# Optimization experiments

Measured on AMD Instinct MI355X. Metric: run time of the kernel, lower is better.

## Reference

```python
import jax, jax.numpy as jnp
import numpy as np

N, D, E, H, O, K = 4096, 1024, 8, 2048, 1024, 2
LOSS_COEF = 0.01


def setup_inputs() -> dict:
    key = jax.random.key(0)
    ks = jax.random.split(key, 8)
    x = jax.random.normal(ks[0], (N, D), jnp.float32)
    return {
        "x": x,
        "x_offsets": jnp.array([0, N // 2, N], jnp.int32),  # unused by forward math
        "max_seq_len": 2048,
        "group_norm": False,
        "num_groups": 8,
        "linear_dim": D // 8,
        "norm_weight": jax.random.uniform(ks[1], (D,), jnp.float32, 0.5, 1.5),
        "norm_bias": jax.random.normal(ks[2], (D,), jnp.float32) * 0.1,
        "norm_eps": 1e-5,
        "w_gate": jax.random.normal(ks[3], (D, E), jnp.float32) * (1.0 / np.sqrt(D)),
        "experts_hidden_w": jax.random.normal(ks[4], (E, H, D), jnp.float32) * 0.02,
        "experts_hidden_bias": jnp.zeros((E, H), jnp.float32),
        "experts_w": jax.random.normal(ks[5], (E, O, H), jnp.float32) * 0.02,
        "experts_bias": jnp.zeros((E, O), jnp.float32),
        "output_weight": jax.random.normal(ks[6], (D, O), jnp.float32) * 0.02,
    }


def _cv_squared(v, eps=1e-6):
    v = v.astype(jnp.float32)
    m = v.mean()
    return jnp.var(v, ddof=1) / (m * m + eps)  # torch .var() is unbiased


def reference(x, x_offsets, max_seq_len, group_norm, num_groups, linear_dim,
              norm_weight, norm_bias, norm_eps,
              w_gate, experts_hidden_w, experts_hidden_bias,
              experts_w, experts_bias, output_weight):
    # ---- input normalization (layer_norm branch; group_norm=False) ----
    if group_norm:
        xg = x.reshape(-1, num_groups, linear_dim)
        mu = xg.mean(axis=2, keepdims=True)
        var = ((xg - mu) ** 2).mean(axis=2, keepdims=True)
        xg = (xg - mu) * jax.lax.rsqrt(var + norm_eps)
        xg = xg * norm_weight[None, :, None] + norm_bias[None, :, None]
        x_norm = xg.reshape(-1, x.shape[-1])
    else:
        mu = x.mean(axis=-1, keepdims=True)
        var = ((x - mu) ** 2).mean(axis=-1, keepdims=True)  # biased, like F.layer_norm
        x_norm = (x - mu) * jax.lax.rsqrt(var + norm_eps) * norm_weight + norm_bias

    # ---- gating: clean logits (enable_noisy_gating=False), L2-normalize rows ----
    logits = x_norm @ w_gate                                  # [N, E]
    logits = logits / jnp.maximum(
        jnp.linalg.norm(logits, axis=1, keepdims=True), 1e-12)
    probs = jax.nn.softmax(logits, axis=1)                    # softmax over all experts
    _, top_idx = jax.lax.top_k(logits, K)                     # [N, K]
    gates_k = jnp.take_along_axis(probs, top_idx, axis=1)     # top-k of softmax(logits)
    rows = jnp.arange(logits.shape[0])[:, None]
    gates = jnp.zeros_like(logits).at[rows, top_idx].set(gates_k)  # [N, E] sparse gates

    # ---- load-balancing loss (train=True, non-noisy path) ----
    importance = gates.sum(axis=0)
    load = (gates > 0).sum(axis=0).astype(jnp.float32)
    loss = (_cv_squared(importance) + _cv_squared(load)) * LOSS_COEF

    # ---- expert MLPs; gates are exactly zero off top-k so masked-dense == dispatch ----
    h = jax.nn.silu(jnp.einsum('nd,ehd->enh', x_norm, experts_hidden_w)
                    + experts_hidden_bias[:, None, :])        # [E, N, H]
    eo = jnp.einsum('enh,eoh->eno', h, experts_w) + experts_bias[:, None, :]  # [E, N, O]
    y_moe = jnp.einsum('ne,eno->no', gates.astype(jnp.float32),
                       eo.astype(jnp.float32))                # fp32 combine, like index_add

    # ---- residual projection: addmm(y_moe, x, output_weight) ----
    y = y_moe + x @ output_weight
    gate_fraction = load / load.sum()
    return (y, loss, gate_fraction)
```

## Files before the change

kernel.cpp:

```cpp
#include <hip/hip_runtime.h>
#include <hip/hip_bf16.h>
#include <stdint.h>

#define N_TOK 4096
#define DIM   1024
#define NE    8
#define NH    2048
#define NO    1024

typedef __attribute__((ext_vector_type(8))) short bf16x8;
typedef __attribute__((ext_vector_type(16))) float f32x16;

__device__ inline unsigned short f2bf(float f) {
    unsigned u = __float_as_uint(f);
    u += 0x7fffu + ((u >> 16) & 1u);
    return (unsigned short)(u >> 16);
}

__device__ inline void async_copy16(const void* g, void* l) {
    __builtin_amdgcn_global_load_lds(
        (const __attribute__((address_space(1))) void*)g,
        (__attribute__((address_space(3))) void*)l, 16, 0, 0);
}

__global__ __launch_bounds__(256) void ln_gate_kernel(
    const float* __restrict__ x, const float* __restrict__ nw,
    const float* __restrict__ nb, const float* __restrict__ eps_p,
    const float* __restrict__ wg,
    unsigned short* __restrict__ xn_bf, unsigned short* __restrict__ x_bf,
    int* __restrict__ tok_e, float* __restrict__ tok_g)
{
    int n = blockIdx.x;
    int t = threadIdx.x;
    int lane = t & 63, wv = t >> 6;

    const float4 xv = ((const float4*)(x + (size_t)n * DIM))[t];
    float s  = xv.x + xv.y + xv.z + xv.w;
    float s2 = xv.x*xv.x + xv.y*xv.y + xv.z*xv.z + xv.w*xv.w;
    #pragma unroll
    for (int o = 32; o > 0; o >>= 1) {
        s  += __shfl_down(s, o);
        s2 += __shfl_down(s2, o);
    }
    __shared__ float rs[4], rs2[4];
    __shared__ float gred[4][NE];
    if (lane == 0) { rs[wv] = s; rs2[wv] = s2; }
    __syncthreads();
    float S  = rs[0] + rs[1] + rs[2] + rs[3];
    float S2 = rs2[0] + rs2[1] + rs2[2] + rs2[3];
    const float inv = 1.0f / (float)DIM;
    float mu = S * inv;
    float var = fmaxf(S2 * inv - mu * mu, 0.0f);
    float rstd = rsqrtf(var + eps_p[0]);

    float4 w4 = ((const float4*)nw)[t];
    float4 b4 = ((const float4*)nb)[t];
    float xn0 = (xv.x - mu) * rstd * w4.x + b4.x;
    float xn1 = (xv.y - mu) * rstd * w4.y + b4.y;
    float xn2 = (xv.z - mu) * rstd * w4.z + b4.z;
    float xn3 = (xv.w - mu) * rstd * w4.w + b4.w;

    ushort4 pn; pn.x = f2bf(xn0); pn.y = f2bf(xn1); pn.z = f2bf(xn2); pn.w = f2bf(xn3);
    ((ushort4*)(xn_bf + (size_t)n * DIM))[t] = pn;
    ushort4 px; px.x = f2bf(xv.x); px.y = f2bf(xv.y); px.z = f2bf(xv.z); px.w = f2bf(xv.w);
    ((ushort4*)(x_bf + (size_t)n * DIM))[t] = px;

    float acc[NE];
    #pragma unroll
    for (int e = 0; e < NE; ++e) acc[e] = 0.0f;
    float xns[4] = {xn0, xn1, xn2, xn3};
    const float4* wgp = (const float4*)(wg + (size_t)(4 * t) * NE);
    #pragma unroll
    for (int j = 0; j < 4; ++j) {
        float4 w0 = wgp[2 * j], w1 = wgp[2 * j + 1];
        float xj = xns[j];
        acc[0] += xj * w0.x; acc[1] += xj * w0.y; acc[2] += xj * w0.z; acc[3] += xj * w0.w;
        acc[4] += xj * w1.x; acc[5] += xj * w1.y; acc[6] += xj * w1.z; acc[7] += xj * w1.w;
    }
    #pragma unroll
    for (int o = 32; o > 0; o >>= 1) {
        #pragma unroll
        for (int e = 0; e < NE; ++e) acc[e] += __shfl_down(acc[e], o);
    }
    if (lane == 0) {
        #pragma unroll
        for (int e = 0; e < NE; ++e) gred[wv][e] = acc[e];
    }
    __syncthreads();
    if (t == 0) {
        float lg[NE];
        float nrm2 = 0.0f;
        #pragma unroll
        for (int e = 0; e < NE; ++e) {
            lg[e] = gred[0][e] + gred[1][e] + gred[2][e] + gred[3][e];
            nrm2 += lg[e] * lg[e];
        }
        float den = fmaxf(sqrtf(nrm2), 1e-12f);
        float linv = 1.0f / den;
        #pragma unroll
        for (int e = 0; e < NE; ++e) lg[e] *= linv;
        float mx = lg[0];
        #pragma unroll
        for (int e = 1; e < NE; ++e) mx = fmaxf(mx, lg[e]);
        float p[NE], ps = 0.0f;
        #pragma unroll
        for (int e = 0; e < NE; ++e) { p[e] = expf(lg[e] - mx); ps += p[e]; }
        float pinv = 1.0f / ps;
        #pragma unroll
        for (int e = 0; e < NE; ++e) p[e] *= pinv;
        int i0 = 0; float b0 = lg[0];
        #pragma unroll
        for (int e = 1; e < NE; ++e) if (lg[e] > b0) { b0 = lg[e]; i0 = e; }
        int i1 = -1; float b1 = -3.0e38f;
        #pragma unroll
        for (int e = 0; e < NE; ++e) if (e != i0 && lg[e] > b1) { b1 = lg[e]; i1 = e; }
        tok_e[2 * n] = i0; tok_e[2 * n + 1] = i1;
        tok_g[2 * n] = p[i0]; tok_g[2 * n + 1] = p[i1];
    }
}

__global__ void cvt2_bf16_kernel(const float* __restrict__ a, unsigned short* __restrict__ da,
                                 const float* __restrict__ b, unsigned short* __restrict__ db,
                                 int n4each) {
    int i = blockIdx.x * blockDim.x + threadIdx.x;
    const float4* s; ushort4* d; int j;
    if (i < n4each) { s = (const float4*)a; d = (ushort4*)da; j = i; }
    else            { s = (const float4*)b; d = (ushort4*)db; j = i - n4each; }
    float4 v = s[j];
    ushort4 o; o.x = f2bf(v.x); o.y = f2bf(v.y); o.z = f2bf(v.z); o.w = f2bf(v.w);
    d[j] = o;
}

__global__ void transpose_cvt_kernel(const float* __restrict__ w,
                                     unsigned short* __restrict__ wt) {
    __shared__ float tile[32][33];
    int tx = threadIdx.x, ty = threadIdx.y;
    int o0 = blockIdx.x * 32, d0 = blockIdx.y * 32;
    tile[ty][tx] = w[(size_t)(d0 + ty) * NO + o0 + tx];
    __syncthreads();
    wt[(size_t)(o0 + ty) * DIM + d0 + tx] = f2bf(tile[tx][ty]);
}

__device__ inline float cv_sq(const float* v) {
    float m = 0.0f;
    for (int e = 0; e < NE; ++e) m += v[e];
    m *= (1.0f / NE);
    float s = 0.0f;
    for (int e = 0; e < NE; ++e) { float d = v[e] - m; s += d * d; }
    s *= (1.0f / (NE - 1));
    return s / (m * m + 1e-6f);
}

__global__ __launch_bounds__(256) void route_kernel(
    const int* __restrict__ tok_e, const float* __restrict__ tok_g,
    int* __restrict__ counts, int* __restrict__ offsets,
    int* __restrict__ rowsbuf, int* __restrict__ pair_slot,
    float* __restrict__ out_tail)
{
    int b = blockIdx.x, t = threadIdx.x;
    int lane = t & 63, wv = t >> 6;
    int chunk0 = b * 1024;

    int lc[NE]; float li[NE];
    #pragma unroll
    for (int e = 0; e < NE; ++e) { lc[e] = 0; li[e] = 0.0f; }
    int base = t * 32;
    #pragma unroll
    for (int q = 0; q < 8; ++q) {
        int4 e4 = *(const int4*)(tok_e + base + q * 4);
        float4 g4 = *(const float4*)(tok_g + base + q * 4);
        lc[e4.x]++; li[e4.x] += g4.x;
        lc[e4.y]++; li[e4.y] += g4.y;
        lc[e4.z]++; li[e4.z] += g4.z;
        lc[e4.w]++; li[e4.w] += g4.w;
    }
    int prior_flag = (base + 32 <= chunk0) ? 1 : 0;
    int lp[NE];
    #pragma unroll
    for (int e = 0; e < NE; ++e) lp[e] = prior_flag ? lc[e] : 0;

    #pragma unroll
    for (int o = 32; o > 0; o >>= 1) {
        #pragma unroll
        for (int e = 0; e < NE; ++e) {
            lc[e] += __shfl_down(lc[e], o);
            lp[e] += __shfl_down(lp[e], o);
            li[e] += __shfl_down(li[e], o);
        }
    }
    __shared__ int   sc[4][NE], sp[4][NE];
    __shared__ float sf[4][NE];
    __shared__ int   lcur[NE];
    if (lane == 0) {
        #pragma unroll
        for (int e = 0; e < NE; ++e) { sc[wv][e] = lc[e]; sp[wv][e] = lp[e]; sf[wv][e] = li[e]; }
    }
    __syncthreads();
    if (t == 0) {
        int cnt[NE], pri[NE]; float imp[NE];
        for (int e = 0; e < NE; ++e) {
            cnt[e] = sc[0][e] + sc[1][e] + sc[2][e] + sc[3][e];
            pri[e] = sp[0][e] + sp[1][e] + sp[2][e] + sp[3][e];
            imp[e] = sf[0][e] + sf[1][e] + sf[2][e] + sf[3][e];
        }
        int off = 0;
        for (int e = 0; e < NE; ++e) {
            lcur[e] = off + pri[e];
            if (b == 0) { counts[e] = cnt[e]; offsets[e] = off; }
            off += cnt[e];
        }
        if (b == 0) {
            float lcf[NE], lif[NE];
            for (int e = 0; e < NE; ++e) { lcf[e] = (float)cnt[e]; lif[e] = imp[e]; }
            float tot = (float)off;
            out_tail[0] = 0.01f * (cv_sq(lif) + cv_sq(lcf));
            for (int e = 0; e < NE; ++e) out_tail[1 + e] = lcf[e] / tot;
        }
    }
    __syncthreads();

    int g0 = chunk0 + 4 * t;
    int4 e4 = *(const int4*)(tok_e + g0);
    int s0 = atomicAdd(&lcur[e4.x], 1);
    int s1 = atomicAdd(&lcur[e4.y], 1);
    int s2 = atomicAdd(&lcur[e4.z], 1);
    int s3 = atomicAdd(&lcur[e4.w], 1);
    int tok0 = g0 >> 1;
    rowsbuf[s0] = tok0;     rowsbuf[s1] = tok0;
    rowsbuf[s2] = tok0 + 1; rowsbuf[s3] = tok0 + 1;
    *(int4*)(pair_slot + g0) = (int4){s0, s1, s2, s3};
}

#define BK 64

__global__ __launch_bounds__(256) void gemm1_kernel(
    const unsigned short* __restrict__ xn,
    const unsigned short* __restrict__ wh,
    const float* __restrict__ hb,
    const int* __restrict__ rowsbuf,
    const int* __restrict__ counts, const int* __restrict__ offsets,
    unsigned short* __restrict__ hbuf)
{
    int e = blockIdx.z;
    int count = counts[e];
    int tm = blockIdx.y, tn = blockIdx.x;
    if (tm * 128 >= count) return;
    int off = offsets[e];

    __shared__ alignas(16) short As[128 * BK];
    __shared__ alignas(16) short Bs[128 * BK];

    int t = threadIdx.x;
    int c = t & 7, rl = t >> 3;
    int csw = (c ^ (rl & 7)) * 8;
    const unsigned short* aptr[4];
    const unsigned short* bptr[4];
    #pragma unroll
    for (int p = 0; p < 4; ++p) {
        int mrow = tm * 128 + p * 32 + rl;
        int mc = mrow < count ? mrow : count - 1;
        int token = rowsbuf[off + mc];
        aptr[p] = xn + (size_t)token * DIM;
        bptr[p] = wh + ((size_t)e * NH + tn * 128 + p * 32 + rl) * DIM;
    }

    int lane = t & 63, wvi = t >> 6;
    int wm = (wvi & 1) * 64, wn = (wvi >> 1) * 64;
    int l31 = lane & 31, h = lane >> 5, sw = l31 & 7;

    f32x16 acc[2][2];
    #pragma unroll
    for (int i = 0; i < 2; ++i)
        #pragma unroll
        for (int j = 0; j < 2; ++j) acc[i][j] = (f32x16)(0.0f);

    for (int kt = 0; kt < DIM / BK; ++kt) {
        int kb = kt * BK + csw;
        #pragma unroll
        for (int p = 0; p < 4; ++p)
            async_copy16(aptr[p] + kb, (char*)As + p * 4096 + t * 16);
        #pragma unroll
        for (int p = 0; p < 4; ++p)
            async_copy16(bptr[p] + kb, (char*)Bs + p * 4096 + t * 16);
        __syncthreads();
        #pragma unroll
        for (int ks = 0; ks < 4; ++ks) {
            int ph = ((ks * 2 + h) ^ sw) * 8;
            bf16x8 af[2], bfr[2];
            #pragma unroll
            for (int i = 0; i < 2; ++i)
                af[i] = *(const bf16x8*)&As[(wm + i * 32 + l31) * BK + ph];
            #pragma unroll
            for (int j = 0; j < 2; ++j)
                bfr[j] = *(const bf16x8*)&Bs[(wn + j * 32 + l31) * BK + ph];
            #pragma unroll
            for (int i = 0; i < 2; ++i)
                #pragma unroll
                for (int j = 0; j < 2; ++j)
                    acc[i][j] = __builtin_amdgcn_mfma_f32_32x32x16_bf16(af[i], bfr[j], acc[i][j], 0, 0, 0);
        }
        __syncthreads();
    }

    #pragma unroll
    for (int i = 0; i < 2; ++i) {
        #pragma unroll
        for (int j = 0; j < 2; ++j) {
            int col = tn * 128 + wn + j * 32 + l31;
            float bias = hb[e * NH + col];
            #pragma unroll
            for (int r = 0; r < 16; ++r) {
                int row_d = (r & 3) + 8 * (r >> 2) + 4 * h;
                int m = tm * 128 + wm + i * 32 + row_d;
                if (m < count) {
                    float v = acc[i][j][r] + bias;
                    v = v / (1.0f + __expf(-v));
                    hbuf[(size_t)(off + m) * NH + col] = f2bf(v);
                }
            }
        }
    }
}

__global__ __launch_bounds__(256) void gemm2_kernel(
    const unsigned short* __restrict__ hbuf,
    const unsigned short* __restrict__ wo,
    const float* __restrict__ ob,
    const int* __restrict__ counts, const int* __restrict__ offsets,
    float* __restrict__ eo)
{
    int e = blockIdx.z;
    int count = counts[e];
    int tm = blockIdx.y, tn = blockIdx.x;
    if (tm * 128 >= count) return;
    int off = offsets[e];

    __shared__ alignas(16) short As[128 * BK];
    __shared__ alignas(16) short Bs[64 * BK];

    int t = threadIdx.x;
    int c = t & 7, rl = t >> 3;
    int csw = (c ^ (rl & 7)) * 8;
    const unsigned short* aptr[4];
    const unsigned short* bptr[2];
    #pragma unroll
    for (int p = 0; p < 4; ++p) {
        int mrow = tm * 128 + p * 32 + rl;
        int mc = mrow < count ? mrow : count - 1;
        aptr[p] = hbuf + (size_t)(off + mc) * NH;
    }
    #pragma unroll
    for (int p = 0; p < 2; ++p)
        bptr[p] = wo + ((size_t)e * NO + tn * 64 + p * 32 + rl) * NH;

    int lane = t & 63, wvi = t >> 6;
    int wm = (wvi & 1) * 64, wn = (wvi >> 1) * 32;
    int l31 = lane & 31, h = lane >> 5, sw = l31 & 7;

    f32x16 acc[2];
    #pragma unroll
    for (int i = 0; i < 2; ++i) acc[i] = (f32x16)(0.0f);

    for (int kt = 0; kt < NH / BK; ++kt) {
        int kb = kt * BK + csw;
        #pragma unroll
        for (int p = 0; p < 4; ++p)
            async_copy16(aptr[p] + kb, (char*)As + p * 4096 + t * 16);
        #pragma unroll
        for (int p = 0; p < 2; ++p)
            async_copy16(bptr[p] + kb, (char*)Bs + p * 4096 + t * 16);
        __syncthreads();
        #pragma unroll
        for (int ks = 0; ks < 4; ++ks) {
            int ph = ((ks * 2 + h) ^ sw) * 8;
            bf16x8 af[2], bfr;
            #pragma unroll
            for (int i = 0; i < 2; ++i)
                af[i] = *(const bf16x8*)&As[(wm + i * 32 + l31) * BK + ph];
            bfr = *(const bf16x8*)&Bs[(wn + l31) * BK + ph];
            #pragma unroll
            for (int i = 0; i < 2; ++i)
                acc[i] = __builtin_amdgcn_mfma_f32_32x32x16_bf16(af[i], bfr, acc[i], 0, 0, 0);
        }
        __syncthreads();
    }

    int col = tn * 64 + wn + l31;
    float bias = ob[e * NO + col];
    #pragma unroll
    for (int i = 0; i < 2; ++i) {
        #pragma unroll
        for (int r = 0; r < 16; ++r) {
            int row_d = (r & 3) + 8 * (r >> 2) + 4 * h;
            int m = tm * 128 + wm + i * 32 + row_d;
            if (m < count)
                eo[(size_t)(off + m) * NO + col] = acc[i][r] + bias;
        }
    }
}

__global__ __launch_bounds__(256) void gemm_res_kernel(
    const unsigned short* __restrict__ xb,
    const unsigned short* __restrict__ wt,
    float* __restrict__ y)
{
    int tm = blockIdx.y, tn = blockIdx.x;
    __shared__ alignas(16) short As[64 * BK];
    __shared__ alignas(16) short Bs[128 * BK];

    int t = threadIdx.x;
    int c = t & 7, rl = t >> 3;
    int csw = (c ^ (rl & 7)) * 8;
    const unsigned short* aptr[2];
    const unsigned short* bptr[4];
    #pragma unroll
    for (int p = 0; p < 2; ++p)
        aptr[p] = xb + (size_t)(tm * 64 + p * 32 + rl) * DIM;
    #pragma unroll
    for (int p = 0; p < 4; ++p)
        bptr[p] = wt + (size_t)(tn * 128 + p * 32 + rl) * DIM;

    int lane = t & 63, wvi = t >> 6;
    int wm = (wvi & 1) * 32, wn = (wvi >> 1) * 64;
    int l31 = lane & 31, h = lane >> 5, sw = l31 & 7;

    f32x16 acc[2];
    #pragma unroll
    for (int j = 0; j < 2; ++j) acc[j] = (f32x16)(0.0f);

    for (int kt = 0; kt < DIM / BK; ++kt) {
        int kb = kt * BK + csw;
        #pragma unroll
        for (int p = 0; p < 2; ++p)
            async_copy16(aptr[p] + kb, (char*)As + p * 4096 + t * 16);
        #pragma unroll
        for (int p = 0; p < 4; ++p)
            async_copy16(bptr[p] + kb, (char*)Bs + p * 4096 + t * 16);
        __syncthreads();
        #pragma unroll
        for (int ks = 0; ks < 4; ++ks) {
            int ph = ((ks * 2 + h) ^ sw) * 8;
            bf16x8 af, bfr[2];
            af = *(const bf16x8*)&As[(wm + l31) * BK + ph];
            #pragma unroll
            for (int j = 0; j < 2; ++j)
                bfr[j] = *(const bf16x8*)&Bs[(wn + j * 32 + l31) * BK + ph];
            #pragma unroll
            for (int j = 0; j < 2; ++j)
                acc[j] = __builtin_amdgcn_mfma_f32_32x32x16_bf16(af, bfr[j], acc[j], 0, 0, 0);
        }
        __syncthreads();
    }

    #pragma unroll
    for (int j = 0; j < 2; ++j) {
        int col = tn * 128 + wn + j * 32 + l31;
        #pragma unroll
        for (int r = 0; r < 16; ++r) {
            int row_d = (r & 3) + 8 * (r >> 2) + 4 * h;
            int row = tm * 64 + wm + row_d;
            y[(size_t)row * NO + col] = acc[j][r];
        }
    }
}

__global__ __launch_bounds__(256) void combine_kernel(
    float* __restrict__ y, const float* __restrict__ eo,
    const int* __restrict__ pair_slot, const float* __restrict__ tok_g)
{
    int n = blockIdx.x, t = threadIdx.x;
    int s0 = pair_slot[2 * n], s1 = pair_slot[2 * n + 1];
    float g0 = tok_g[2 * n], g1 = tok_g[2 * n + 1];
    float4 a = ((const float4*)(eo + (size_t)s0 * NO))[t];
    float4 b = ((const float4*)(eo + (size_t)s1 * NO))[t];
    float4* yp = (float4*)(y + (size_t)n * NO) + t;
    float4 v = *yp;
    v.x += g0 * a.x + g1 * b.x;
    v.y += g0 * a.y + g1 * b.y;
    v.z += g0 * a.z + g1 * b.z;
    v.w += g0 * a.w + g1 * b.w;
    *yp = v;
}

extern "C" void kernel_launch(void* const* d_in, const int* in_sizes, int n_in,
                              void* d_out, int out_size, void* d_ws, size_t ws_size,
                              hipStream_t stream) {
    const float* x    = (const float*)d_in[0];
    const float* nw   = (const float*)d_in[6];
    const float* nb   = (const float*)d_in[7];
    const float* eps  = (const float*)d_in[8];
    const float* wg   = (const float*)d_in[9];
    const float* whw  = (const float*)d_in[10];
    const float* whb  = (const float*)d_in[11];
    const float* wow  = (const float*)d_in[12];
    const float* wob  = (const float*)d_in[13];
    const float* wout = (const float*)d_in[14];

    char* ws = (char*)d_ws;
    unsigned short* xn_bf = (unsigned short*)(ws + 0);
    unsigned short* x_bf  = (unsigned short*)(ws + 8388608);
    unsigned short* wh_bf = (unsigned short*)(ws + 16777216);
    float*          eo    = (float*)(ws + 16777216);
    unsigned short* wo_bf = (unsigned short*)(ws + 50331648);
    unsigned short* wt_bf = (unsigned short*)(ws + 83886080);
    unsigned short* hbuf  = (unsigned short*)(ws + 85983232);
    char* meta = ws + 119537664;
    int*   counts     = (int*)(meta + 0);
    int*   offsets    = (int*)(meta + 128);
    int*   tok_e      = (int*)(meta + 2048);
    float* tok_g      = (float*)(meta + 2048 + 32768);
    int*   rowsbuf    = (int*)(meta + 2048 + 65536);
    int*   pair_slot  = (int*)(meta + 2048 + 98304);

    float* y = (float*)d_out;
    float* out_tail = y + (size_t)N_TOK * NO;

    ln_gate_kernel<<<N_TOK, 256, 0, stream>>>(x, nw, nb, eps, wg, xn_bf, x_bf,
                                              tok_e, tok_g);
    {
        int n4 = NE * NH * DIM / 4;
        cvt2_bf16_kernel<<<2 * n4 / 256, 256, 0, stream>>>(whw, wh_bf, wow, wo_bf, n4);
    }
    transpose_cvt_kernel<<<dim3(NO / 32, DIM / 32), dim3(32, 32), 0, stream>>>(wout, wt_bf);
    route_kernel<<<NE, 256, 0, stream>>>(tok_e, tok_g, counts, offsets,
                                         rowsbuf, pair_slot, out_tail);
    gemm1_kernel<<<dim3(NH / 128, N_TOK / 128, NE), 256, 0, stream>>>(
        xn_bf, wh_bf, whb, rowsbuf, counts, offsets, hbuf);
    gemm2_kernel<<<dim3(NO / 64, N_TOK / 128, NE), 256, 0, stream>>>(
        hbuf, wo_bf, wob, counts, offsets, eo);
    gemm_res_kernel<<<dim3(NO / 128, N_TOK / 64), 256, 0, stream>>>(x_bf, wt_bf, y);
    combine_kernel<<<N_TOK, 256, 0, stream>>>(y, eo, pair_slot, tok_g);
}
```

Measured before the change: 389.1 us.

## Fuse prep kernels and scatter gated expert outputs via atomics into y

Merges the weight conversion, transpose, and routing kernels into one prep launch. Moves the residual GEMM ahead of the expert GEMMs so that gemm2 can add gate-weighted outputs straight into y with float atomics. This removes the fp32 eo buffer round trip and the separate combine kernel. The cost is 8M scattered atomic adds, and the fp32 summation order becomes nondeterministic.

```diff
diff --git a/kernel.cpp b/kernel.cpp
--- a/kernel.cpp
+++ b/kernel.cpp
@@ -119,28 +119,6 @@
     }
 }
 
-__global__ void cvt2_bf16_kernel(const float* __restrict__ a, unsigned short* __restrict__ da,
-                                 const float* __restrict__ b, unsigned short* __restrict__ db,
-                                 int n4each) {
-    int i = blockIdx.x * blockDim.x + threadIdx.x;
-    const float4* s; ushort4* d; int j;
-    if (i < n4each) { s = (const float4*)a; d = (ushort4*)da; j = i; }
-    else            { s = (const float4*)b; d = (ushort4*)db; j = i - n4each; }
-    float4 v = s[j];
-    ushort4 o; o.x = f2bf(v.x); o.y = f2bf(v.y); o.z = f2bf(v.z); o.w = f2bf(v.w);
-    d[j] = o;
-}
-
-__global__ void transpose_cvt_kernel(const float* __restrict__ w,
-                                     unsigned short* __restrict__ wt) {
-    __shared__ float tile[32][33];
-    int tx = threadIdx.x, ty = threadIdx.y;
-    int o0 = blockIdx.x * 32, d0 = blockIdx.y * 32;
-    tile[ty][tx] = w[(size_t)(d0 + ty) * NO + o0 + tx];
-    __syncthreads();
-    wt[(size_t)(o0 + ty) * DIM + d0 + tx] = f2bf(tile[tx][ty]);
-}
-
 __device__ inline float cv_sq(const float* v) {
     float m = 0.0f;
     for (int e = 0; e < NE; ++e) m += v[e];
@@ -151,15 +129,55 @@
     return s / (m * m + 1e-6f);
 }
 
-__global__ __launch_bounds__(256) void route_kernel(
+#define CVT_BLK 32768
+__global__ __launch_bounds__(256) void prep_kernel(
+    const float* __restrict__ whw, unsigned short* __restrict__ wh_bf,
+    const float* __restrict__ wow, unsigned short* __restrict__ wo_bf,
+    const float* __restrict__ wout, unsigned short* __restrict__ wt_bf,
     const int* __restrict__ tok_e, const float* __restrict__ tok_g,
     int* __restrict__ counts, int* __restrict__ offsets,
-    int* __restrict__ rowsbuf, int* __restrict__ pair_slot,
+    int* __restrict__ rowsbuf, float* __restrict__ gatebuf,
     float* __restrict__ out_tail)
 {
+    __shared__ float tile[32][33];
+    __shared__ int   sc[4][NE], sp[4][NE];
+    __shared__ float sf[4][NE];
+    __shared__ int   lcur[NE];
+
     int b = blockIdx.x, t = threadIdx.x;
+
+    if (b < CVT_BLK) {
+        const int n4each = NE * NH * DIM / 4;
+        int i = b * 256 + t;
+        const float4* s; ushort4* d; int j;
+        if (i < n4each) { s = (const float4*)whw; d = (ushort4*)wh_bf; j = i; }
+        else            { s = (const float4*)wow; d = (ushort4*)wo_bf; j = i - n4each; }
+        float4 v = s[j];
+        ushort4 o; o.x = f2bf(v.x); o.y = f2bf(v.y); o.z = f2bf(v.z); o.w = f2bf(v.w);
+        d[j] = o;
+        return;
+    }
+    if (b < CVT_BLK + 1024) {
+        int idx = b - CVT_BLK;
+        int o0 = (idx & 31) * 32, d0 = (idx >> 5) * 32;
+        int tx = t & 31, ty0 = t >> 5;
+        #pragma unroll
+        for (int k = 0; k < 4; ++k) {
+            int ty = ty0 + k * 8;
+            tile[ty][tx] = wout[(size_t)(d0 + ty) * NO + o0 + tx];
+        }
+        __syncthreads();
+        #pragma unroll
+        for (int k = 0; k < 4; ++k) {
+            int ty = ty0 + k * 8;
+            wt_bf[(size_t)(o0 + ty) * DIM + d0 + tx] = f2bf(tile[tx][ty]);
+        }
+        return;
+    }
+
+    int rb = b - (CVT_BLK + 1024);
     int lane = t & 63, wv = t >> 6;
-    int chunk0 = b * 1024;
+    int chunk0 = rb * 1024;
 
     int lc[NE]; float li[NE];
     #pragma unroll
@@ -188,9 +206,6 @@
             li[e] += __shfl_down(li[e], o);
         }
     }
-    __shared__ int   sc[4][NE], sp[4][NE];
-    __shared__ float sf[4][NE];
-    __shared__ int   lcur[NE];
     if (lane == 0) {
         #pragma unroll
         for (int e = 0; e < NE; ++e) { sc[wv][e] = lc[e]; sp[wv][e] = lp[e]; sf[wv][e] = li[e]; }
@@ -206,10 +221,10 @@
         int off = 0;
         for (int e = 0; e < NE; ++e) {
             lcur[e] = off + pri[e];
-            if (b == 0) { counts[e] = cnt[e]; offsets[e] = off; }
+            if (rb == 0) { counts[e] = cnt[e]; offsets[e] = off; }
             off += cnt[e];
         }
-        if (b == 0) {
+        if (rb == 0) {
             float lcf[NE], lif[NE];
             for (int e = 0; e < NE; ++e) { lcf[e] = (float)cnt[e]; lif[e] = imp[e]; }
             float tot = (float)off;
@@ -221,6 +236,7 @@
 
     int g0 = chunk0 + 4 * t;
     int4 e4 = *(const int4*)(tok_e + g0);
+    float4 g4 = *(const float4*)(tok_g + g0);
     int s0 = atomicAdd(&lcur[e4.x], 1);
     int s1 = atomicAdd(&lcur[e4.y], 1);
     int s2 = atomicAdd(&lcur[e4.z], 1);
@@ -228,7 +244,8 @@
     int tok0 = g0 >> 1;
     rowsbuf[s0] = tok0;     rowsbuf[s1] = tok0;
     rowsbuf[s2] = tok0 + 1; rowsbuf[s3] = tok0 + 1;
-    *(int4*)(pair_slot + g0) = (int4){s0, s1, s2, s3};
+    gatebuf[s0] = g4.x; gatebuf[s1] = g4.y;
+    gatebuf[s2] = g4.z; gatebuf[s3] = g4.w;
 }
 
 #define BK 64
@@ -327,7 +344,8 @@
     const unsigned short* __restrict__ wo,
     const float* __restrict__ ob,
     const int* __restrict__ counts, const int* __restrict__ offsets,
-    float* __restrict__ eo)
+    const int* __restrict__ rowsbuf, const float* __restrict__ gatebuf,
+    float* __restrict__ y)
 {
     int e = blockIdx.z;
     int count = counts[e];
@@ -393,8 +411,14 @@
         for (int r = 0; r < 16; ++r) {
             int row_d = (r & 3) + 8 * (r >> 2) + 4 * h;
             int m = tm * 128 + wm + i * 32 + row_d;
-            if (m < count)
-                eo[(size_t)(off + m) * NO + col] = acc[i][r] + bias;
+            if (m < count) {
+                int slot = off + m;
+                int token = rowsbuf[slot];
+                float g = gatebuf[slot];
+                __hip_atomic_fetch_add(&y[(size_t)token * NO + col],
+                                       g * (acc[i][r] + bias),
+                                       __ATOMIC_RELAXED, __HIP_MEMORY_SCOPE_AGENT);
+            }
         }
     }
 }
@@ -462,24 +486,6 @@
             y[(size_t)row * NO + col] = acc[j][r];
         }
     }
-}
-
-__global__ __launch_bounds__(256) void combine_kernel(
-    float* __restrict__ y, const float* __restrict__ eo,
-    const int* __restrict__ pair_slot, const float* __restrict__ tok_g)
-{
-    int n = blockIdx.x, t = threadIdx.x;
-    int s0 = pair_slot[2 * n], s1 = pair_slot[2 * n + 1];
-    float g0 = tok_g[2 * n], g1 = tok_g[2 * n + 1];
-    float4 a = ((const float4*)(eo + (size_t)s0 * NO))[t];
-    float4 b = ((const float4*)(eo + (size_t)s1 * NO))[t];
-    float4* yp = (float4*)(y + (size_t)n * NO) + t;
-    float4 v = *yp;
-    v.x += g0 * a.x + g1 * b.x;
-    v.y += g0 * a.y + g1 * b.y;
-    v.z += g0 * a.z + g1 * b.z;
-    v.w += g0 * a.w + g1 * b.w;
-    *yp = v;
 }
 
 extern "C" void kernel_launch(void* const* d_in, const int* in_sizes, int n_in,
@@ -500,7 +506,6 @@
     unsigned short* xn_bf = (unsigned short*)(ws + 0);
     unsigned short* x_bf  = (unsigned short*)(ws + 8388608);
     unsigned short* wh_bf = (unsigned short*)(ws + 16777216);
-    float*          eo    = (float*)(ws + 16777216);
     unsigned short* wo_bf = (unsigned short*)(ws + 50331648);
     unsigned short* wt_bf = (unsigned short*)(ws + 83886080);
     unsigned short* hbuf  = (unsigned short*)(ws + 85983232);
@@ -510,24 +515,19 @@
     int*   tok_e      = (int*)(meta + 2048);
     float* tok_g      = (float*)(meta + 2048 + 32768);
     int*   rowsbuf    = (int*)(meta + 2048 + 65536);
-    int*   pair_slot  = (int*)(meta + 2048 + 98304);
+    float* gatebuf    = (float*)(meta + 2048 + 98304);
 
     float* y = (float*)d_out;
     float* out_tail = y + (size_t)N_TOK * NO;
 
     ln_gate_kernel<<<N_TOK, 256, 0, stream>>>(x, nw, nb, eps, wg, xn_bf, x_bf,
                                               tok_e, tok_g);
-    {
-        int n4 = NE * NH * DIM / 4;
-        cvt2_bf16_kernel<<<2 * n4 / 256, 256, 0, stream>>>(whw, wh_bf, wow, wo_bf, n4);
-    }
-    transpose_cvt_kernel<<<dim3(NO / 32, DIM / 32), dim3(32, 32), 0, stream>>>(wout, wt_bf);
-    route_kernel<<<NE, 256, 0, stream>>>(tok_e, tok_g, counts, offsets,
-                                         rowsbuf, pair_slot, out_tail);
+    prep_kernel<<<CVT_BLK + 1024 + 8, 256, 0, stream>>>(
+        whw, wh_bf, wow, wo_bf, wout, wt_bf,
+        tok_e, tok_g, counts, offsets, rowsbuf, gatebuf, out_tail);
+    gemm_res_kernel<<<dim3(NO / 128, N_TOK / 64), 256, 0, stream>>>(x_bf, wt_bf, y);
     gemm1_kernel<<<dim3(NH / 128, N_TOK / 128, NE), 256, 0, stream>>>(
         xn_bf, wh_bf, whb, rowsbuf, counts, offsets, hbuf);
     gemm2_kernel<<<dim3(NO / 64, N_TOK / 128, NE), 256, 0, stream>>>(
-        hbuf, wo_bf, wob, counts, offsets, eo);
-    gemm_res_kernel<<<dim3(NO / 128, N_TOK / 64), 256, 0, stream>>>(x_bf, wt_bf, y);
-    combine_kernel<<<N_TOK, 256, 0, stream>>>(y, eo, pair_slot, tok_g);
-}
+        hbuf, wo_bf, wob, counts, offsets, rowsbuf, gatebuf, y);
+}
```

Result: no change. 383.4 us (-1.5%).
